# Kernel tuning notes

Hardware: AMD Instinct MI355X
Metric: run time of the kernel (lower is better)

## Reference

```python
import jax, jax.numpy as jnp
import numpy as np

SEGMENT_LENGTHS = [2048, 4096, 8192]
DILATION_RATES = [1, 2, 4]
RING_SIZE = 4


def _head_groups(h, g):
    base, rem = divmod(h, g)
    return [base + (1 if i < rem else 0) for i in range(g)]


def _dilation_pattern(n, seg, r, group_idx):
    # Per-segment dilated index pattern of total length n (index_select target).
    s = min(seg, n)
    off = group_idx % r
    base = (off + np.arange(0, s, r)) % s          # stride-r indices within segment
    pat_seg = np.tile(base, r)[:s]                  # repeat to fill segment length
    nseg = n // s
    pat = (pat_seg[None, :] + np.arange(nseg)[:, None] * s).reshape(-1)
    return pat


def _apply_dilation(x):
    # x: (b, n, h, d). Gather along sequence per head group.
    b, n, h, d = x.shape
    groups = _head_groups(h, len(SEGMENT_LENGTHS))
    outs, hs = [], 0
    for i, (seg, r, g) in enumerate(zip(SEGMENT_LENGTHS, DILATION_RATES, groups)):
        if g == 0:
            continue
        pat = jnp.asarray(_dilation_pattern(n, seg, r, i))
        outs.append(x[:, pat, hs:hs + g, :])
        hs += g
    return jnp.concatenate(outs, axis=2)


def setup_inputs() -> dict:
    key = jax.random.key(0)
    k1, k2, k3 = jax.random.split(key, 3)
    shape = (1, 8192, 16, 64)
    return {
        "q": jax.random.normal(k1, shape, dtype=jnp.float32),
        "k": jax.random.normal(k2, shape, dtype=jnp.float32),
        "v": jax.random.normal(k3, shape, dtype=jnp.float32),
    }


def reference(q, k, v):
    b, n, h, d = q.shape
    scale = 1.0 / jnp.sqrt(jnp.asarray(d, q.dtype))
    chunk = n // RING_SIZE

    # Dilate queries once; dilate each local KV chunk (ring-distributed layout).
    qt = _apply_dilation(q).transpose(0, 2, 1, 3)   # (b, h, n, d)

    acc_out = jnp.zeros((b, h, n, d), q.dtype)
    acc_lse = jnp.full((b, h, n), -jnp.inf, q.dtype)

    # Simulated ring pass: iterate over KV chunks with online-LSE accumulation.
    for c in range(RING_SIZE):
        kc = _apply_dilation(k[:, c * chunk:(c + 1) * chunk])  # (b, chunk, h, d)
        vc = _apply_dilation(v[:, c * chunk:(c + 1) * chunk])
        scores = jnp.einsum('bhqd,bkhd->bhqk', qt, kc) * scale
        lse_c = jax.nn.logsumexp(scores, axis=-1)              # (b, h, n)
        out_c = jnp.einsum('bhqk,bkhd->bhqd',
                           jax.nn.softmax(scores, axis=-1), vc)
        new_lse = jnp.logaddexp(acc_lse, lse_c)
        w_old = jnp.exp(acc_lse - new_lse)[..., None]
        w_new = jnp.exp(lse_c - new_lse)[..., None]
        acc_out = w_old * acc_out + w_new * out_c
        acc_lse = new_lse

    return acc_out.transpose(0, 2, 1, 3)  # (b, n, h, d)
```

## Files before the change

### kernel.cpp

```cpp
#include <hip/hip_runtime.h>
#include <hip/hip_bf16.h>
#include <math.h>

typedef __attribute__((ext_vector_type(4))) float f32x4;
typedef __attribute__((ext_vector_type(8))) short bf16x8;
typedef __attribute__((ext_vector_type(4))) short s16x4;

#define NH 16
#define HD 64
#define BM 128
#define BM2 256
#define BN 64
#define WM 32
#define LDS_K 72
#define TILE_B 18432
#define TILE_S 9216

#define OPART4_OFF 23003136ull
#define LPART4_OFF (OPART4_OFF + 25165824ull)
#define WS4_NEEDED (LPART4_OFF + 393216ull)

__device__ __forceinline__ short f2bf(float f) {
    union { float f; unsigned u; } x; x.f = f;
    unsigned r = x.u + 0x7fffu + ((x.u >> 16) & 1u);
    return (short)(r >> 16);
}
__device__ __forceinline__ unsigned pack2bf(float a, float b) {
    union { float f; unsigned u; } x, y; x.f = a; y.f = b;
    return __builtin_amdgcn_perm(y.u + 0x8000u, x.u + 0x8000u, 0x07060302u);
}
__device__ __forceinline__ float elem(const float4& r, int j) {
    return ((const float*)&r)[j];
}
__device__ __forceinline__ size_t head_base(int h) {
    if (h < 6)  return (size_t)h * (128 * TILE_B);
    if (h < 11) return 6ull * (128 * TILE_B) + (size_t)(h - 6) * (64 * TILE_B);
    return 6ull * (128 * TILE_B) + 5ull * (64 * TILE_B) + (size_t)(h - 11) * (32 * TILE_B);
}

__global__ __launch_bounds__(256)
void rda_pack(const float* __restrict__ K, const float* __restrict__ V, char* __restrict__ W) {
    int bid = blockIdx.x;
    int h, t, type;
    if (bid < 768)       { type = 0; h = bid >> 7;                t = bid & 127; }
    else if (bid < 1088) { type = 1; h = 6 + ((bid - 768) >> 6);  t = (bid - 768) & 63; }
    else                 { type = 2; h = 11 + ((bid - 1088) >> 5); t = (bid - 1088) & 31; }
    int rate = 1 << type, off = type;
    char* tile = W + head_base(h) + (size_t)t * TILE_B;
    int tid = threadIdx.x;
    {
        int row = tid >> 2, c = (tid & 3) * 16;
        int pos = rate * (t * 64 + row) + off;
        const float* p = K + ((size_t)pos * NH + h) * HD + c;
        float4 a0 = ((const float4*)p)[0], a1 = ((const float4*)p)[1];
        float4 a2 = ((const float4*)p)[2], a3 = ((const float4*)p)[3];
        uint4 d0, d1;
        d0.x = pack2bf(elem(a0,0), elem(a0,1)); d0.y = pack2bf(elem(a0,2), elem(a0,3));
        d0.z = pack2bf(elem(a1,0), elem(a1,1)); d0.w = pack2bf(elem(a1,2), elem(a1,3));
        d1.x = pack2bf(elem(a2,0), elem(a2,1)); d1.y = pack2bf(elem(a2,2), elem(a2,3));
        d1.z = pack2bf(elem(a3,0), elem(a3,1)); d1.w = pack2bf(elem(a3,2), elem(a3,3));
        char* dst = tile + row * (LDS_K * 2) + c * 2;
        ((uint4*)dst)[0] = d0;
        ((uint4*)dst)[1] = d1;
    }
    {
        int vr = (tid & 15) * 4, vc = (tid >> 4) * 4;
        float4 vv[4];
#pragma unroll
        for (int i = 0; i < 4; ++i) {
            int pos = rate * (t * 64 + vr + i) + off;
            vv[i] = *(const float4*)(V + ((size_t)pos * NH + h) * HD + vc);
        }
#pragma unroll
        for (int j = 0; j < 4; ++j) {
            uint2 w;
            w.x = pack2bf(elem(vv[0], j), elem(vv[1], j));
            w.y = pack2bf(elem(vv[2], j), elem(vv[3], j));
            *(uint2*)(tile + 9216 + (vc + j) * (LDS_K * 2) + vr * 2) = w;
        }
    }
}

__global__ __launch_bounds__(512, 4)
void rda_attn_w8(const float* __restrict__ Q, char* __restrict__ W, float* __restrict__ O) {
    __shared__ __align__(16) short sKV[2 * TILE_S];
    __shared__ __align__(16) short sP[8][WM * 64];

    int bid = blockIdx.x;
    int h, mb, type, kc, nst, sid;
    if (bid < 384)      { type = 0; h = bid >> 6; int rem = bid & 63; mb = rem >> 1; kc = rem & 1; nst = 64; sid = bid; }
    else if (bid < 464) { type = 1; int rel = bid - 384; h = 6 + (rel >> 4); mb = rel & 15; kc = 0; nst = 64; sid = -1; }
    else                { type = 2; int rel = bid - 464; h = 11 + (rel >> 3); mb = rel & 7; kc = 0; nst = 32; sid = -1; }
    int rate = 1 << type;
    int off  = type;
    int kb0  = kc * 64;

    int tid  = threadIdx.x;
    int wave = tid >> 6;
    int lane = tid & 63;
    int ln   = lane & 15;
    int quad = lane >> 4;

    const float SC = 0.125f * 1.4426950408889634f;

    int qbase = mb * BM2 + wave * WM;
    bf16x8 qf[2][2];
#pragma unroll
    for (int mt = 0; mt < 2; ++mt) {
        int u = qbase + mt * 16 + ln;
        size_t base = ((size_t)(rate * u + off) * NH + h) * HD;
#pragma unroll
        for (int ks = 0; ks < 2; ++ks) {
            const float* p = Q + base + ks * 32 + quad * 8;
            float4 a = ((const float4*)p)[0];
            float4 b = ((const float4*)p)[1];
            union { uint4 u4; bf16x8 f; } cv;
            cv.u4.x = pack2bf(elem(a,0)*SC, elem(a,1)*SC);
            cv.u4.y = pack2bf(elem(a,2)*SC, elem(a,3)*SC);
            cv.u4.z = pack2bf(elem(b,0)*SC, elem(b,1)*SC);
            cv.u4.w = pack2bf(elem(b,2)*SC, elem(b,3)*SC);
            qf[mt][ks] = cv.f;
        }
    }

    f32x4 acc[2][4];
#pragma unroll
    for (int mt = 0; mt < 2; ++mt)
#pragma unroll
        for (int dt = 0; dt < 4; ++dt) acc[mt][dt] = (f32x4){0.f, 0.f, 0.f, 0.f};
    float lp[2] = {0.f, 0.f};

    const char* gh = W + head_base(h);

    auto stage = [&](const char* gt, int lB) {
#pragma unroll
        for (int r = 0; r < 2; ++r) {
            int c = r * 8192 + tid * 16;
            __builtin_amdgcn_global_load_lds(
                (const __attribute__((address_space(1))) unsigned*)(gt + c),
                (__attribute__((address_space(3))) unsigned*)((char*)sKV + lB + c),
                16, 0, 0);
        }
        if (tid < 128) {
            int c = 16384 + tid * 16;
            __builtin_amdgcn_global_load_lds(
                (const __attribute__((address_space(1))) unsigned*)(gt + c),
                (__attribute__((address_space(3))) unsigned*)((char*)sKV + lB + c),
                16, 0, 0);
        }
    };

    stage(gh + (size_t)kb0 * TILE_B, 0);
    int pB = 0;

    char* pbase = (char*)&sP[wave][0];

    for (int i = 0; i < nst; ++i) {
        int kb = kb0 + i;
        __syncthreads();

        if (i + 1 < nst) stage(gh + (size_t)(kb + 1) * TILE_B, pB ^ TILE_B);

        const short* sK  = (const short*)((const char*)sKV + pB);
        const short* sVT = sK + BN * LDS_K;

        f32x4 st[4][2];
        __builtin_amdgcn_s_setprio(1);
#pragma unroll
        for (int kt = 0; kt < 4; ++kt) {
            bf16x8 a0 = *(bf16x8*)&sK[(kt * 16 + ln) * LDS_K + quad * 8];
            bf16x8 a1 = *(bf16x8*)&sK[(kt * 16 + ln) * LDS_K + 32 + quad * 8];
#pragma unroll
            for (int mt = 0; mt < 2; ++mt) {
                f32x4 c = (f32x4){0.f, 0.f, 0.f, 0.f};
                c = __builtin_amdgcn_mfma_f32_16x16x32_bf16(a0, qf[mt][0], c, 0, 0, 0);
                c = __builtin_amdgcn_mfma_f32_16x16x32_bf16(a1, qf[mt][1], c, 0, 0, 0);
                st[kt][mt] = c;
            }
        }
        __builtin_amdgcn_s_setprio(0);

#pragma unroll
        for (int mt = 0; mt < 2; ++mt)
#pragma unroll
            for (int kt = 0; kt < 4; ++kt) {
                float p0 = __builtin_amdgcn_exp2f(st[kt][mt][0]);
                float p1 = __builtin_amdgcn_exp2f(st[kt][mt][1]);
                float p2 = __builtin_amdgcn_exp2f(st[kt][mt][2]);
                float p3 = __builtin_amdgcn_exp2f(st[kt][mt][3]);
                st[kt][mt][0] = p0; st[kt][mt][1] = p1;
                st[kt][mt][2] = p2; st[kt][mt][3] = p3;
                lp[mt] += (p0 + p1) + (p2 + p3);
            }

#pragma unroll
        for (int mt = 0; mt < 2; ++mt)
#pragma unroll
            for (int kt = 0; kt < 4; ++kt) {
                uint2 pk;
                pk.x = pack2bf(st[kt][mt][0], st[kt][mt][1]);
                pk.y = pack2bf(st[kt][mt][2], st[kt][mt][3]);
                int prow = mt * 16 + ln;
                int pbyte = (prow * 128 + (kt * 16 + quad * 4) * 2) ^ ((prow & 7) << 4);
                *(uint2*)(pbase + pbyte) = pk;
            }
        __asm__ volatile("s_waitcnt lgkmcnt(0)" ::: "memory");

        __builtin_amdgcn_s_setprio(1);
#pragma unroll
        for (int ksk = 0; ksk < 2; ++ksk) {
            int b0 = (ln * 128 + (ksk * 32 + quad * 8) * 2) ^ ((ln & 7) << 4);
            int b1 = ((16 + ln) * 128 + (ksk * 32 + quad * 8) * 2) ^ ((ln & 7) << 4);
            bf16x8 pa0 = *(bf16x8*)(pbase + b0);
            bf16x8 pa1 = *(bf16x8*)(pbase + b1);
#pragma unroll
            for (int dt = 0; dt < 4; ++dt) {
                bf16x8 vb = *(bf16x8*)&sVT[(dt * 16 + ln) * LDS_K + ksk * 32 + quad * 8];
                acc[0][dt] = __builtin_amdgcn_mfma_f32_16x16x32_bf16(pa0, vb, acc[0][dt], 0, 0, 0);
                acc[1][dt] = __builtin_amdgcn_mfma_f32_16x16x32_bf16(pa1, vb, acc[1][dt], 0, 0, 0);
            }
        }
        __builtin_amdgcn_s_setprio(0);
        pB ^= TILE_B;
    }

#pragma unroll
    for (int mt = 0; mt < 2; ++mt) {
        lp[mt] += __shfl_xor(lp[mt], 16);
        lp[mt] += __shfl_xor(lp[mt], 32);
    }

    if (type == 0) {
        float* Op = (float*)(W + OPART4_OFF) + (size_t)sid * (BM2 * HD);
        float* Lp = (float*)(W + LPART4_OFF) + (size_t)sid * BM2;
#pragma unroll
        for (int mt = 0; mt < 2; ++mt) {
            if (quad == 0) Lp[wave * WM + mt * 16 + ln] = lp[mt];
#pragma unroll
            for (int r = 0; r < 4; ++r) {
                int ql = wave * WM + mt * 16 + quad * 4 + r;
#pragma unroll
                for (int dt = 0; dt < 4; ++dt)
                    Op[ql * HD + dt * 16 + ln] = acc[mt][dt][r];
            }
        }
    } else {
#pragma unroll
        for (int mt = 0; mt < 2; ++mt)
#pragma unroll
            for (int r = 0; r < 4; ++r) {
                float lO = __shfl(lp[mt], quad * 4 + r);
                float inv = 1.0f / lO;
                int u = qbase + mt * 16 + quad * 4 + r;
#pragma unroll
                for (int dt = 0; dt < 4; ++dt) {
                    float val = acc[mt][dt][r] * inv;
                    int dcol = dt * 16 + ln;
                    if (type == 1) {
                        int r0 = ((u >> 11) << 12) + (u & 2047);
                        O[((size_t)r0 * NH + h) * HD + dcol] = val;
                        O[((size_t)(r0 + 2048) * NH + h) * HD + dcol] = val;
                    } else {
#pragma unroll
                        for (int t = 0; t < 4; ++t)
                            O[((size_t)(u + t * 2048) * NH + h) * HD + dcol] = val;
                    }
                }
            }
    }
}

__global__ __launch_bounds__(256)
void rda_comb4(const char* __restrict__ W, float* __restrict__ O) {
    int c = blockIdx.x;
    int h = c >> 5, mb = c & 31;
    int s0 = c * 2;

    const float* P0 = (const float*)(W + OPART4_OFF) + (size_t)s0 * (BM2 * HD);
    const float* L0 = (const float*)(W + LPART4_OFF) + (size_t)s0 * BM2;

    __shared__ float sInv[BM2];
    int tid = threadIdx.x;
    sInv[tid] = 1.0f / (L0[tid] + L0[BM2 + tid]);
    __syncthreads();

#pragma unroll
    for (int i = 0; i < 16; ++i) {
        int f = i * 256 + tid;
        int q = f >> 4, d4 = f & 15;
        float4 a = ((const float4*)P0)[f];
        float4 b = ((const float4*)(P0 + BM2 * HD))[f];
        float inv = sInv[q];
        float4 v;
        v.x = (a.x + b.x) * inv; v.y = (a.y + b.y) * inv;
        v.z = (a.z + b.z) * inv; v.w = (a.w + b.w) * inv;
        int u = mb * BM2 + q;
        *(float4*)&O[((size_t)u * NH + h) * HD + d4 * 4] = v;
    }
}

__global__ __launch_bounds__(256, 2)
void rda_attn_fb(const float* __restrict__ Q, const float* __restrict__ K,
                 const float* __restrict__ V, float* __restrict__ O) {
    __shared__ short sK[BN * LDS_K];
    __shared__ short sVT[HD * LDS_K];
    __shared__ short sP[4][WM * LDS_K];

    int bid = blockIdx.x;
    int h, mb, type;
    if (bid < 384)      { type = 0; h = bid >> 6;               mb = bid & 63; }
    else if (bid < 544) { type = 1; h = 6 + ((bid - 384) >> 5); mb = (bid - 384) & 31; }
    else                { type = 2; h = 11 + ((bid - 544) >> 4); mb = (bid - 544) & 15; }
    int rate = 1 << type;
    int off  = type;
    int nsteps = 128 >> type;

    int tid  = threadIdx.x;
    int wave = tid >> 6;
    int lane = tid & 63;
    int ln   = lane & 15;
    int quad = lane >> 4;

    const float SC = 0.125f * 1.4426950408889634f;

    int qbase = mb * BM + wave * WM;
    bf16x8 qf[2][2];
#pragma unroll
    for (int mt = 0; mt < 2; ++mt) {
        int u = qbase + mt * 16 + ln;
        size_t base = ((size_t)(rate * u + off) * NH + h) * HD;
#pragma unroll
        for (int ks = 0; ks < 2; ++ks) {
            const float* p = Q + base + ks * 32 + quad * 8;
            float4 a = ((const float4*)p)[0];
            float4 b = ((const float4*)p)[1];
            bf16x8 f;
#pragma unroll
            for (int i = 0; i < 4; ++i) { f[i] = f2bf(elem(a, i) * SC); f[4 + i] = f2bf(elem(b, i) * SC); }
            qf[mt][ks] = f;
        }
    }

    f32x4 acc[2][4];
#pragma unroll
    for (int mt = 0; mt < 2; ++mt)
#pragma unroll
        for (int dt = 0; dt < 4; ++dt) acc[mt][dt] = (f32x4){0.f, 0.f, 0.f, 0.f};
    float m_i[2] = {-INFINITY, -INFINITY};
    float l_i[2] = {0.f, 0.f};

    int srow = tid >> 2, sc0 = (tid & 3) * 16;
    int vr = (tid >> 4) * 4, vc = (tid & 15) * 4;

    for (int kb = 0; kb < nsteps; ++kb) {
        {
            int kpos = rate * (kb * BN + srow) + off;
            const float* p = K + ((size_t)kpos * NH + h) * HD + sc0;
            float4 kv0 = ((const float4*)p)[0], kv1 = ((const float4*)p)[1];
            float4 kv2 = ((const float4*)p)[2], kv3 = ((const float4*)p)[3];
            bf16x8 f0, f1;
#pragma unroll
            for (int i = 0; i < 4; ++i) {
                f0[i] = f2bf(elem(kv0, i)); f0[4 + i] = f2bf(elem(kv1, i));
                f1[i] = f2bf(elem(kv2, i)); f1[4 + i] = f2bf(elem(kv3, i));
            }
            *(bf16x8*)&sK[srow * LDS_K + sc0] = f0;
            *(bf16x8*)&sK[srow * LDS_K + sc0 + 8] = f1;
        }
        {
            float4 vv[4];
#pragma unroll
            for (int i = 0; i < 4; ++i) {
                int kpos = rate * (kb * BN + vr + i) + off;
                vv[i] = *(const float4*)(V + ((size_t)kpos * NH + h) * HD + vc);
            }
#pragma unroll
            for (int j = 0; j < 4; ++j) {
                s16x4 t;
                t[0] = f2bf(elem(vv[0], j)); t[1] = f2bf(elem(vv[1], j));
                t[2] = f2bf(elem(vv[2], j)); t[3] = f2bf(elem(vv[3], j));
                *(s16x4*)&sVT[(vc + j) * LDS_K + vr] = t;
            }
        }
        __syncthreads();

        f32x4 st[4][2];
#pragma unroll
        for (int kt = 0; kt < 4; ++kt) {
            bf16x8 a0 = *(bf16x8*)&sK[(kt * 16 + ln) * LDS_K + quad * 8];
            bf16x8 a1 = *(bf16x8*)&sK[(kt * 16 + ln) * LDS_K + 32 + quad * 8];
#pragma unroll
            for (int mt = 0; mt < 2; ++mt) {
                f32x4 c = (f32x4){0.f, 0.f, 0.f, 0.f};
                c = __builtin_amdgcn_mfma_f32_16x16x32_bf16(a0, qf[mt][0], c, 0, 0, 0);
                c = __builtin_amdgcn_mfma_f32_16x16x32_bf16(a1, qf[mt][1], c, 0, 0, 0);
                st[kt][mt] = c;
            }
        }

#pragma unroll
        for (int mt = 0; mt < 2; ++mt) {
            float tmax = -INFINITY;
#pragma unroll
            for (int kt = 0; kt < 4; ++kt)
#pragma unroll
                for (int r = 0; r < 4; ++r) tmax = fmaxf(tmax, st[kt][mt][r]);
            tmax = fmaxf(tmax, __shfl_xor(tmax, 16));
            tmax = fmaxf(tmax, __shfl_xor(tmax, 32));
            float mnew = fmaxf(m_i[mt], tmax);
            float al = exp2f(m_i[mt] - mnew);
            m_i[mt] = mnew;
            float rs = 0.f;
#pragma unroll
            for (int kt = 0; kt < 4; ++kt)
#pragma unroll
                for (int r = 0; r < 4; ++r) {
                    float pe = exp2f(st[kt][mt][r] - mnew);
                    st[kt][mt][r] = pe;
                    rs += pe;
                }
            rs += __shfl_xor(rs, 16);
            rs += __shfl_xor(rs, 32);
            l_i[mt] = l_i[mt] * al + rs;
#pragma unroll
            for (int r = 0; r < 4; ++r) {
                float aO = __shfl(al, quad * 4 + r);
#pragma unroll
                for (int dt = 0; dt < 4; ++dt) acc[mt][dt][r] *= aO;
            }
        }

#pragma unroll
        for (int mt = 0; mt < 2; ++mt)
#pragma unroll
            for (int kt = 0; kt < 4; ++kt) {
                s16x4 pk;
                pk[0] = f2bf(st[kt][mt][0]); pk[1] = f2bf(st[kt][mt][1]);
                pk[2] = f2bf(st[kt][mt][2]); pk[3] = f2bf(st[kt][mt][3]);
                *(s16x4*)&sP[wave][(mt * 16 + ln) * LDS_K + kt * 16 + quad * 4] = pk;
            }
        __asm__ volatile("s_waitcnt lgkmcnt(0)" ::: "memory");

#pragma unroll
        for (int ksk = 0; ksk < 2; ++ksk) {
            bf16x8 pa0 = *(bf16x8*)&sP[wave][(ln) * LDS_K + ksk * 32 + quad * 8];
            bf16x8 pa1 = *(bf16x8*)&sP[wave][(16 + ln) * LDS_K + ksk * 32 + quad * 8];
#pragma unroll
            for (int dt = 0; dt < 4; ++dt) {
                bf16x8 vb = *(bf16x8*)&sVT[(dt * 16 + ln) * LDS_K + ksk * 32 + quad * 8];
                acc[0][dt] = __builtin_amdgcn_mfma_f32_16x16x32_bf16(pa0, vb, acc[0][dt], 0, 0, 0);
                acc[1][dt] = __builtin_amdgcn_mfma_f32_16x16x32_bf16(pa1, vb, acc[1][dt], 0, 0, 0);
            }
        }
        __syncthreads();
    }

#pragma unroll
    for (int mt = 0; mt < 2; ++mt) {
#pragma unroll
        for (int r = 0; r < 4; ++r) {
            float lO = __shfl(l_i[mt], quad * 4 + r);
            float inv = 1.0f / lO;
            int u = qbase + mt * 16 + quad * 4 + r;
#pragma unroll
            for (int dt = 0; dt < 4; ++dt) {
                float val = acc[mt][dt][r] * inv;
                int dcol = dt * 16 + ln;
                if (type == 0) {
                    O[((size_t)u * NH + h) * HD + dcol] = val;
                } else if (type == 1) {
                    int r0 = ((u >> 11) << 12) + (u & 2047);
                    O[((size_t)r0 * NH + h) * HD + dcol] = val;
                    O[((size_t)(r0 + 2048) * NH + h) * HD + dcol] = val;
                } else {
#pragma unroll
                    for (int t = 0; t < 4; ++t)
                        O[((size_t)(u + t * 2048) * NH + h) * HD + dcol] = val;
                }
            }
        }
    }
}

extern "C" void kernel_launch(void* const* d_in, const int* in_sizes, int n_in,
                              void* d_out, int out_size, void* d_ws, size_t ws_size,
                              hipStream_t stream) {
    (void)in_sizes; (void)n_in; (void)out_size;
    const float* q = (const float*)d_in[0];
    const float* k = (const float*)d_in[1];
    const float* v = (const float*)d_in[2];
    float* o = (float*)d_out;
    if (ws_size >= WS4_NEEDED && d_ws != nullptr) {
        rda_pack<<<dim3(1248), dim3(256), 0, stream>>>(k, v, (char*)d_ws);
        rda_attn_w8<<<dim3(504), dim3(512), 0, stream>>>(q, (char*)d_ws, o);
        rda_comb4<<<dim3(192), dim3(256), 0, stream>>>((const char*)d_ws, o);
    } else {
        rda_attn_fb<<<dim3(624), dim3(256), 0, stream>>>(q, k, v, o);
    }
}
```

Measured before the change: 286.3 us.

## Replace padded KV tiles with XOR-swizzled layout and split P staging into halves

The packed K and V^T tiles switch from padded 72-element rows to unpadded 64-element rows with an XOR swizzle, which shrinks each tile from 18432 to 16384 bytes and lets the async global-to-LDS staging drop its extra partial load. The attention loop now handles each 64-key tile as two 32-key halves, so the per-wave P buffer in LDS is halved and the score tile held in registers is smaller. The aims are less LDS footprint and traffic, fewer bank conflicts, and lower register pressure, at the cost of more swizzle address arithmetic and an extra waitcnt per half-tile.

```diff
diff --git a/kernel.cpp b/kernel.cpp
--- a/kernel.cpp
+++ b/kernel.cpp
@@ -13,12 +13,12 @@
 #define BN 64
 #define WM 32
 #define LDS_K 72
-#define TILE_B 18432
-#define TILE_S 9216
-
-#define OPART4_OFF 23003136ull
-#define LPART4_OFF (OPART4_OFF + 25165824ull)
-#define WS4_NEEDED (LPART4_OFF + 393216ull)
+#define TILE2_B 16384
+#define WS_FB 0ull
+
+#define OPART5_OFF 20447232ull
+#define LPART5_OFF (OPART5_OFF + 25165824ull)
+#define WS5_NEEDED (LPART5_OFF + 393216ull)
 
 __device__ __forceinline__ short f2bf(float f) {
     union { float f; unsigned u; } x; x.f = f;
@@ -32,21 +32,21 @@
 __device__ __forceinline__ float elem(const float4& r, int j) {
     return ((const float*)&r)[j];
 }
-__device__ __forceinline__ size_t head_base(int h) {
-    if (h < 6)  return (size_t)h * (128 * TILE_B);
-    if (h < 11) return 6ull * (128 * TILE_B) + (size_t)(h - 6) * (64 * TILE_B);
-    return 6ull * (128 * TILE_B) + 5ull * (64 * TILE_B) + (size_t)(h - 11) * (32 * TILE_B);
+__device__ __forceinline__ size_t head_base2(int h) {
+    if (h < 6)  return (size_t)h * (128 * TILE2_B);
+    if (h < 11) return 6ull * (128 * TILE2_B) + (size_t)(h - 6) * (64 * TILE2_B);
+    return 6ull * (128 * TILE2_B) + 5ull * (64 * TILE2_B) + (size_t)(h - 11) * (32 * TILE2_B);
 }
 
 __global__ __launch_bounds__(256)
-void rda_pack(const float* __restrict__ K, const float* __restrict__ V, char* __restrict__ W) {
+void rda_pack2(const float* __restrict__ K, const float* __restrict__ V, char* __restrict__ W) {
     int bid = blockIdx.x;
     int h, t, type;
     if (bid < 768)       { type = 0; h = bid >> 7;                t = bid & 127; }
     else if (bid < 1088) { type = 1; h = 6 + ((bid - 768) >> 6);  t = (bid - 768) & 63; }
     else                 { type = 2; h = 11 + ((bid - 1088) >> 5); t = (bid - 1088) & 31; }
     int rate = 1 << type, off = type;
-    char* tile = W + head_base(h) + (size_t)t * TILE_B;
+    char* tile = W + head_base2(h) + (size_t)t * TILE2_B;
     int tid = threadIdx.x;
     {
         int row = tid >> 2, c = (tid & 3) * 16;
@@ -59,9 +59,10 @@
         d0.z = pack2bf(elem(a1,0), elem(a1,1)); d0.w = pack2bf(elem(a1,2), elem(a1,3));
         d1.x = pack2bf(elem(a2,0), elem(a2,1)); d1.y = pack2bf(elem(a2,2), elem(a2,3));
         d1.z = pack2bf(elem(a3,0), elem(a3,1)); d1.w = pack2bf(elem(a3,2), elem(a3,3));
-        char* dst = tile + row * (LDS_K * 2) + c * 2;
-        ((uint4*)dst)[0] = d0;
-        ((uint4*)dst)[1] = d1;
+        int L = row * 128 + c * 2;
+        int sw = (row & 7) << 4;
+        *(uint4*)(tile + (L ^ sw)) = d0;
+        *(uint4*)(tile + ((L + 16) ^ sw)) = d1;
     }
     {
         int vr = (tid & 15) * 4, vc = (tid >> 4) * 4;
@@ -76,15 +77,17 @@
             uint2 w;
             w.x = pack2bf(elem(vv[0], j), elem(vv[1], j));
             w.y = pack2bf(elem(vv[2], j), elem(vv[3], j));
-            *(uint2*)(tile + 9216 + (vc + j) * (LDS_K * 2) + vr * 2) = w;
+            int rr = vc + j;
+            int L = rr * 128 + vr * 2;
+            *(uint2*)(tile + 8192 + (L ^ ((rr & 7) << 4))) = w;
         }
     }
 }
 
 __global__ __launch_bounds__(512, 4)
-void rda_attn_w8(const float* __restrict__ Q, char* __restrict__ W, float* __restrict__ O) {
-    __shared__ __align__(16) short sKV[2 * TILE_S];
-    __shared__ __align__(16) short sP[8][WM * 64];
+void rda_attn_w8s(const float* __restrict__ Q, char* __restrict__ W, float* __restrict__ O) {
+    __shared__ __align__(16) short sKV[2 * 8192];
+    __shared__ __align__(16) short sP[8][1024];
 
     int bid = blockIdx.x;
     int h, mb, type, kc, nst, sid;
@@ -130,7 +133,7 @@
         for (int dt = 0; dt < 4; ++dt) acc[mt][dt] = (f32x4){0.f, 0.f, 0.f, 0.f};
     float lp[2] = {0.f, 0.f};
 
-    const char* gh = W + head_base(h);
+    const char* gh = W + head_base2(h);
 
     auto stage = [&](const char* gt, int lB) {
 #pragma unroll
@@ -141,16 +144,9 @@
                 (__attribute__((address_space(3))) unsigned*)((char*)sKV + lB + c),
                 16, 0, 0);
         }
-        if (tid < 128) {
-            int c = 16384 + tid * 16;
-            __builtin_amdgcn_global_load_lds(
-                (const __attribute__((address_space(1))) unsigned*)(gt + c),
-                (__attribute__((address_space(3))) unsigned*)((char*)sKV + lB + c),
-                16, 0, 0);
-        }
     };
 
-    stage(gh + (size_t)kb0 * TILE_B, 0);
+    stage(gh + (size_t)kb0 * TILE2_B, 0);
     int pB = 0;
 
     char* pbase = (char*)&sP[wave][0];
@@ -159,69 +155,64 @@
         int kb = kb0 + i;
         __syncthreads();
 
-        if (i + 1 < nst) stage(gh + (size_t)(kb + 1) * TILE_B, pB ^ TILE_B);
-
-        const short* sK  = (const short*)((const char*)sKV + pB);
-        const short* sVT = sK + BN * LDS_K;
-
-        f32x4 st[4][2];
-        __builtin_amdgcn_s_setprio(1);
-#pragma unroll
-        for (int kt = 0; kt < 4; ++kt) {
-            bf16x8 a0 = *(bf16x8*)&sK[(kt * 16 + ln) * LDS_K + quad * 8];
-            bf16x8 a1 = *(bf16x8*)&sK[(kt * 16 + ln) * LDS_K + 32 + quad * 8];
-#pragma unroll
-            for (int mt = 0; mt < 2; ++mt) {
-                f32x4 c = (f32x4){0.f, 0.f, 0.f, 0.f};
-                c = __builtin_amdgcn_mfma_f32_16x16x32_bf16(a0, qf[mt][0], c, 0, 0, 0);
-                c = __builtin_amdgcn_mfma_f32_16x16x32_bf16(a1, qf[mt][1], c, 0, 0, 0);
-                st[kt][mt] = c;
-            }
-        }
-        __builtin_amdgcn_s_setprio(0);
-
-#pragma unroll
-        for (int mt = 0; mt < 2; ++mt)
-#pragma unroll
-            for (int kt = 0; kt < 4; ++kt) {
-                float p0 = __builtin_amdgcn_exp2f(st[kt][mt][0]);
-                float p1 = __builtin_amdgcn_exp2f(st[kt][mt][1]);
-                float p2 = __builtin_amdgcn_exp2f(st[kt][mt][2]);
-                float p3 = __builtin_amdgcn_exp2f(st[kt][mt][3]);
-                st[kt][mt][0] = p0; st[kt][mt][1] = p1;
-                st[kt][mt][2] = p2; st[kt][mt][3] = p3;
-                lp[mt] += (p0 + p1) + (p2 + p3);
-            }
-
-#pragma unroll
-        for (int mt = 0; mt < 2; ++mt)
-#pragma unroll
-            for (int kt = 0; kt < 4; ++kt) {
-                uint2 pk;
-                pk.x = pack2bf(st[kt][mt][0], st[kt][mt][1]);
-                pk.y = pack2bf(st[kt][mt][2], st[kt][mt][3]);
-                int prow = mt * 16 + ln;
-                int pbyte = (prow * 128 + (kt * 16 + quad * 4) * 2) ^ ((prow & 7) << 4);
-                *(uint2*)(pbase + pbyte) = pk;
-            }
-        __asm__ volatile("s_waitcnt lgkmcnt(0)" ::: "memory");
-
-        __builtin_amdgcn_s_setprio(1);
-#pragma unroll
-        for (int ksk = 0; ksk < 2; ++ksk) {
-            int b0 = (ln * 128 + (ksk * 32 + quad * 8) * 2) ^ ((ln & 7) << 4);
-            int b1 = ((16 + ln) * 128 + (ksk * 32 + quad * 8) * 2) ^ ((ln & 7) << 4);
+        if (i + 1 < nst) stage(gh + (size_t)(kb + 1) * TILE2_B, pB ^ TILE2_B);
+
+        const char* sKb = (const char*)sKV + pB;
+        const char* sVb = sKb + 8192;
+
+#pragma unroll
+        for (int x = 0; x < 2; ++x) {
+            f32x4 st[2][2];
+            __builtin_amdgcn_s_setprio(1);
+#pragma unroll
+            for (int kk = 0; kk < 2; ++kk) {
+                int ra = (2 * x + kk) * 16 + ln;
+                int sw = (ra & 7) << 4;
+                bf16x8 a0 = *(const bf16x8*)(sKb + ((ra * 128 + quad * 16) ^ sw));
+                bf16x8 a1 = *(const bf16x8*)(sKb + ((ra * 128 + 64 + quad * 16) ^ sw));
+#pragma unroll
+                for (int mt = 0; mt < 2; ++mt) {
+                    f32x4 c = (f32x4){0.f, 0.f, 0.f, 0.f};
+                    c = __builtin_amdgcn_mfma_f32_16x16x32_bf16(a0, qf[mt][0], c, 0, 0, 0);
+                    c = __builtin_amdgcn_mfma_f32_16x16x32_bf16(a1, qf[mt][1], c, 0, 0, 0);
+                    st[kk][mt] = c;
+                }
+            }
+            __builtin_amdgcn_s_setprio(0);
+
+#pragma unroll
+            for (int mt = 0; mt < 2; ++mt)
+#pragma unroll
+                for (int kk = 0; kk < 2; ++kk) {
+                    float p0 = __builtin_amdgcn_exp2f(st[kk][mt][0]);
+                    float p1 = __builtin_amdgcn_exp2f(st[kk][mt][1]);
+                    float p2 = __builtin_amdgcn_exp2f(st[kk][mt][2]);
+                    float p3 = __builtin_amdgcn_exp2f(st[kk][mt][3]);
+                    lp[mt] += (p0 + p1) + (p2 + p3);
+                    uint2 pk;
+                    pk.x = pack2bf(p0, p1);
+                    pk.y = pack2bf(p2, p3);
+                    int prow = mt * 16 + ln;
+                    int Lb = prow * 64 + kk * 32 + quad * 8;
+                    *(uint2*)(pbase + (Lb ^ (((prow >> 1) & 3) << 4))) = pk;
+                }
+            __asm__ volatile("s_waitcnt lgkmcnt(0)" ::: "memory");
+
+            __builtin_amdgcn_s_setprio(1);
+            int b0 = (ln * 64 + quad * 16) ^ (((ln >> 1) & 3) << 4);
+            int b1 = ((16 + ln) * 64 + quad * 16) ^ ((((16 + ln) >> 1) & 3) << 4);
             bf16x8 pa0 = *(bf16x8*)(pbase + b0);
             bf16x8 pa1 = *(bf16x8*)(pbase + b1);
 #pragma unroll
             for (int dt = 0; dt < 4; ++dt) {
-                bf16x8 vb = *(bf16x8*)&sVT[(dt * 16 + ln) * LDS_K + ksk * 32 + quad * 8];
+                int rv = dt * 16 + ln;
+                bf16x8 vb = *(const bf16x8*)(sVb + ((rv * 128 + x * 64 + quad * 16) ^ ((rv & 7) << 4)));
                 acc[0][dt] = __builtin_amdgcn_mfma_f32_16x16x32_bf16(pa0, vb, acc[0][dt], 0, 0, 0);
                 acc[1][dt] = __builtin_amdgcn_mfma_f32_16x16x32_bf16(pa1, vb, acc[1][dt], 0, 0, 0);
             }
-        }
-        __builtin_amdgcn_s_setprio(0);
-        pB ^= TILE_B;
+            __builtin_amdgcn_s_setprio(0);
+        }
+        pB ^= TILE2_B;
     }
 
 #pragma unroll
@@ -231,8 +222,8 @@
     }
 
     if (type == 0) {
-        float* Op = (float*)(W + OPART4_OFF) + (size_t)sid * (BM2 * HD);
-        float* Lp = (float*)(W + LPART4_OFF) + (size_t)sid * BM2;
+        float* Op = (float*)(W + OPART5_OFF) + (size_t)sid * (BM2 * HD);
+        float* Lp = (float*)(W + LPART5_OFF) + (size_t)sid * BM2;
 #pragma unroll
         for (int mt = 0; mt < 2; ++mt) {
             if (quad == 0) Lp[wave * WM + mt * 16 + ln] = lp[mt];
@@ -271,13 +262,13 @@
 }
 
 __global__ __launch_bounds__(256)
-void rda_comb4(const char* __restrict__ W, float* __restrict__ O) {
+void rda_comb5(const char* __restrict__ W, float* __restrict__ O) {
     int c = blockIdx.x;
     int h = c >> 5, mb = c & 31;
     int s0 = c * 2;
 
-    const float* P0 = (const float*)(W + OPART4_OFF) + (size_t)s0 * (BM2 * HD);
-    const float* L0 = (const float*)(W + LPART4_OFF) + (size_t)s0 * BM2;
+    const float* P0 = (const float*)(W + OPART5_OFF) + (size_t)s0 * (BM2 * HD);
+    const float* L0 = (const float*)(W + LPART5_OFF) + (size_t)s0 * BM2;
 
     __shared__ float sInv[BM2];
     int tid = threadIdx.x;
@@ -490,10 +481,10 @@
     const float* k = (const float*)d_in[1];
     const float* v = (const float*)d_in[2];
     float* o = (float*)d_out;
-    if (ws_size >= WS4_NEEDED && d_ws != nullptr) {
-        rda_pack<<<dim3(1248), dim3(256), 0, stream>>>(k, v, (char*)d_ws);
-        rda_attn_w8<<<dim3(504), dim3(512), 0, stream>>>(q, (char*)d_ws, o);
-        rda_comb4<<<dim3(192), dim3(256), 0, stream>>>((const char*)d_ws, o);
+    if (ws_size >= WS5_NEEDED && d_ws != nullptr) {
+        rda_pack2<<<dim3(1248), dim3(256), 0, stream>>>(k, v, (char*)d_ws);
+        rda_attn_w8s<<<dim3(504), dim3(512), 0, stream>>>(q, (char*)d_ws, o);
+        rda_comb5<<<dim3(192), dim3(256), 0, stream>>>((const char*)d_ws, o);
     } else {
         rda_attn_fb<<<dim3(624), dim3(256), 0, stream>>>(q, k, v, o);
     }
```

After: 293.0 us. 1.02x slower.
